# Optimization experiments

Hardware: AMD Instinct MI355X
Metric: run time of the kernel (lower is better)

The kernel has to match this reference:

```python
import jax, jax.numpy as jnp
import numpy as np

B, L, G, HID, H, D = 2, 4096, 256, 768, 12, 64
R = 127            # local_radius
BLK = R + 1        # block_len = 128
N = L // BLK       # 32 blocks (L divisible by BLK)
W = 2 * R + 1      # 255 local window
V = 32             # relative vocab size


def setup_inputs() -> dict:
    ks = jax.random.split(jax.random.key(0), 40)
    inp = {}
    inp["long_input"] = jax.random.normal(ks[0], (B, L, HID), jnp.float32)
    inp["global_input"] = jax.random.normal(ks[1], (B, G, HID), jnp.float32)
    inp["l2l_att_mask"] = jax.random.randint(ks[2], (B, L, W), 0, 2, jnp.int32)
    inp["g2g_att_mask"] = jax.random.randint(ks[3], (B, G, G), 0, 2, jnp.int32)
    inp["l2g_att_mask"] = jax.random.randint(ks[4], (B, L, G), 0, 2, jnp.int32)
    inp["g2l_att_mask"] = jax.random.randint(ks[5], (B, G, L), 0, 2, jnp.int32)
    inp["l2l_relative_att_ids"] = jax.random.randint(ks[6], (B, L, W), 0, V, jnp.int32)
    inp["g2g_relative_att_ids"] = jax.random.randint(ks[7], (B, G, G), 0, V, jnp.int32)
    inp["l2g_relative_att_ids"] = jax.random.randint(ks[8], (B, L, G), 0, V, jnp.int32)
    inp["g2l_relative_att_ids"] = jax.random.randint(ks[9], (B, G, L), 0, V, jnp.int32)
    i = 10
    for nm in ["q_long", "k_long", "v_long", "q_glob", "k_glob", "v_glob"]:
        inp["w" + nm] = 0.02 * jax.random.normal(ks[i], (HID, H * D), jnp.float32); i += 1
        inp["b" + nm] = jnp.zeros((H * D,), jnp.float32)
    inp["rel_emb_long"] = 0.5 * jax.random.normal(ks[i], (V, H, D), jnp.float32); i += 1
    inp["rel_bias_long"] = jnp.zeros((V, H), jnp.float32)
    inp["rel_emb_glob"] = 0.5 * jax.random.normal(ks[i], (V, H, D), jnp.float32); i += 1
    inp["rel_bias_glob"] = jnp.zeros((V, H), jnp.float32)
    inp["wo_long"] = 0.02 * jax.random.normal(ks[i], (H * D, HID), jnp.float32); i += 1
    inp["bo_long"] = jnp.zeros((HID,), jnp.float32)
    inp["wo_glob"] = 0.02 * jax.random.normal(ks[i], (H * D, HID), jnp.float32); i += 1
    inp["bo_glob"] = jnp.zeros((HID,), jnp.float32)
    return inp


def _expand_local(x):
    """[B, L, W] local-window ids -> blocked [B, N, BLK, 3*BLK] (skew + pad),
    zeroing entries outside the local window or outside the sequence."""
    xb = x.reshape(B, N, BLK, W)
    p = jnp.arange(BLK)[:, None]        # query pos within block
    c = jnp.arange(3 * BLK)[None, :]    # key pos within 3-block window
    r = c - p - 1                       # index into the 2R+1 window
    valid = (r >= 0) & (r < W)
    rc = jnp.clip(r, 0, W - 1)
    out = jnp.take_along_axis(xb, jnp.broadcast_to(rc, (B, N, BLK, 3 * BLK)), axis=-1)
    j = (jnp.arange(N)[:, None, None] - 1) * BLK + c  # absolute key position
    valid_full = valid[None] & (j >= 0) & (j < L)     # [N, BLK, 3*BLK]
    return out * valid_full[None].astype(x.dtype)


def reference(long_input, global_input,
              l2l_att_mask, g2g_att_mask, l2g_att_mask, g2l_att_mask,
              l2l_relative_att_ids, g2g_relative_att_ids,
              l2g_relative_att_ids, g2l_relative_att_ids,
              wq_long, bq_long, wk_long, bk_long, wv_long, bv_long,
              wq_glob, bq_glob, wk_glob, bk_glob, wv_glob, bv_glob,
              rel_emb_long, rel_bias_long, rel_emb_glob, rel_bias_glob,
              wo_long, bo_long, wo_glob, bo_glob):
    scale = 1.0 / jnp.sqrt(jnp.float32(D))

    def proj(x, w, b):
        return (x @ w + b).reshape(x.shape[0], x.shape[1], H, D)

    lq, lk, lv = proj(long_input, wq_long, bq_long), proj(long_input, wk_long, bk_long), proj(long_input, wv_long, bv_long)
    gq, gk, gv = proj(global_input, wq_glob, bq_glob), proj(global_input, wk_glob, bk_glob), proj(global_input, wv_glob, bv_glob)

    # ---- long tokens: blocked local attention fused with side (global) keys ----
    qb = lq.reshape(B, N, BLK, H, D)

    def concat3(x):
        xb = x.reshape(B, N, BLK, H, D)
        pad = jnp.zeros_like(xb[:, :1])
        xp = jnp.concatenate([pad, xb, pad], axis=1)  # [B, N+2, BLK, H, D]
        return jnp.concatenate([xp[:, :-2], xp[:, 1:-1], xp[:, 2:]], axis=2)  # [B,N,3BLK,H,D]

    keys = jnp.concatenate([concat3(lk), jnp.broadcast_to(gk[:, None], (B, N, G, H, D))], axis=2)
    vals = jnp.concatenate([concat3(lv), jnp.broadcast_to(gv[:, None], (B, N, G, H, D))], axis=2)

    mask = jnp.concatenate([_expand_local(l2l_att_mask), l2g_att_mask.reshape(B, N, BLK, G)], axis=-1)
    ids = jnp.concatenate([_expand_local(l2l_relative_att_ids), l2g_relative_att_ids.reshape(B, N, BLK, G)], axis=-1)

    scores = jnp.einsum('bnqhd,bnkhd->bnqkh', qb, keys)
    rel_all = jnp.einsum('bnqhd,rhd->bnqrh', qb, rel_emb_long) + rel_bias_long
    rel = jnp.take_along_axis(rel_all, jnp.broadcast_to(ids[..., None], ids.shape + (H,)), axis=3)
    scores = (scores + rel) * scale
    scores = scores - 10000.0 * (1.0 - mask[..., None].astype(scores.dtype))
    probs = jax.nn.softmax(scores, axis=3)
    long_ctx = jnp.einsum('bnqkh,bnkhd->bnqhd', probs, vals).reshape(B, L, H * D)
    long_out = long_ctx @ wo_long + bo_long

    # ---- global tokens: full attention over [global; long] keys ----
    kf = jnp.concatenate([gk, lk], axis=1)
    vf = jnp.concatenate([gv, lv], axis=1)
    gmask = jnp.concatenate([g2g_att_mask, g2l_att_mask], axis=-1)
    gids = jnp.concatenate([g2g_relative_att_ids, g2l_relative_att_ids], axis=-1)
    gs = jnp.einsum('bqhd,bkhd->bqkh', gq, kf)
    grel_all = jnp.einsum('bqhd,rhd->bqrh', gq, rel_emb_glob) + rel_bias_glob
    grel = jnp.take_along_axis(grel_all, jnp.broadcast_to(gids[..., None], gids.shape + (H,)), axis=2)
    gs = (gs + grel) * scale
    gs = gs - 10000.0 * (1.0 - gmask[..., None].astype(gs.dtype))
    gp = jax.nn.softmax(gs, axis=2)
    glob_ctx = jnp.einsum('bqkh,bkhd->bqhd', gp, vf).reshape(B, G, H * D)
    glob_out = glob_ctx @ wo_glob + bo_glob

    return long_out, glob_out
```

## Files before the change

kernel.cpp:

```cpp
#include <hip/hip_runtime.h>
#include <hip/hip_bf16.h>

typedef unsigned short u16;
typedef unsigned char u8;
typedef unsigned int u32;
typedef __attribute__((ext_vector_type(8))) short bf16x8;
typedef __attribute__((ext_vector_type(4))) float f32x4;

#define BB 2
#define LL 4096
#define GG 256
#define HH 12
#define DD 64
#define NB 32
#define WW 255
#define VV 32
#define NCHUNK 17
#define LKEY 640
#define GKEY 4352
#define WMAT 589824
#define MMAT 294912

#define PKL_BLK 20480
#define PKG_BLK 8704
#define WPR_BLK 1152
#define XPL_BLK 3072
#define XPG_BLK 192
#define MPR_BLK 768

__device__ __forceinline__ float bf2f(u16 u) {
  return __uint_as_float(((unsigned)u) << 16);
}
__device__ __forceinline__ u16 f2bf(float f) {
  unsigned u = __float_as_uint(f);
  u += 0x7FFFu + ((u >> 16) & 1u);
  return (u16)(u >> 16);
}
__device__ __forceinline__ float4 ld4bf(const u16* p) {
  ushort4 q = *reinterpret_cast<const ushort4*>(p);
  return make_float4(bf2f(q.x), bf2f(q.y), bf2f(q.z), bf2f(q.w));
}
__device__ __forceinline__ float ldx1(const void* p, size_t idx, bool f32m) {
  if (f32m) return reinterpret_cast<const float*>(p)[idx];
// ... 26 lines not shown
          const int* __restrict__ m_g2g, const int* __restrict__ m_g2l,
          const int* __restrict__ i_g2g, const int* __restrict__ i_g2l,
          u8* __restrict__ pkl, u8* __restrict__ pkg,
          const void* __restrict__ W0, const void* __restrict__ W1,
          const void* __restrict__ W2, const void* __restrict__ W3,
          const void* __restrict__ W4, const void* __restrict__ W5,
          const void* __restrict__ W6, const void* __restrict__ W7,
          u16* __restrict__ wtq, u16* __restrict__ wto,
          const void* __restrict__ xlin, const void* __restrict__ xgin,
          u16* __restrict__ xl, u16* __restrict__ xg,
          const void* __restrict__ embl, const void* __restrict__ rbl,
          const void* __restrict__ embg, const void* __restrict__ rbg,
          const void* __restrict__ bql, const void* __restrict__ bqg,
          u16* __restrict__ wtrel, float* __restrict__ crel,
          const int* __restrict__ flagp) {
  __shared__ u16 T[64][72];
  const bool f32m = (*flagp != 0);
  const int tid = threadIdx.x;
  const int bid = blockIdx.x;

  if (bid < PKL_BLK) {
    const unsigned idx = (unsigned)bid * 256u + tid;
    const int pos = idx & 63;
    const int lnp = pos >> 2, ktp = pos & 3;
    const int qrow = (idx >> 6) & 127;
    const unsigned rest = idx >> 13;
    const int tile = rest % 10;
    const unsigned bn = rest / 10;
    const int n = bn & 31, b = bn >> 5;
    const int c = (tile << 6) + (ktp << 4) + lnp;
    const unsigned bt = (unsigned)b * LL + (n << 7) + qrow;
// ... 19 lines not shown
    const int tl = rest % 68;
    const unsigned b2q = rest / 68;
    const int b = b2q >> 1, qtp = b2q & 1;
    const int c = (tl << 6) + (ktp << 4) + lnp;
    const int q = (qtp << 7) + qrow;
    int mask, id;
    if (c < 256) {
      const size_t base = ((size_t)b * GG + q) * GG + c;
      mask = m_g2g[base]; id = i_g2g[base];
    } else {
      const size_t base = ((size_t)b * GG + q) * (size_t)LL + (c - 256);
      mask = m_g2l[base]; id = i_g2l[base];
    }
    pkg[idx] = (u8)((id & 31) | ((mask ^ 1) << 7));
  } else if (bid < PKL_BLK + PKG_BLK + WPR_BLK) {
    const int blk = bid - (PKL_BLK + PKG_BLK);
    const int mat = blk / 144;
    const int rem = blk % 144;
    const int n0 = (rem % 12) << 6, k0 = (rem / 12) << 6;
    const void* Wm = (mat == 0) ? W0 : (mat == 1) ? W1 : (mat == 2) ? W2
                     : (mat == 3) ? W3 : (mat == 4) ? W4 : (mat == 5) ? W5
                     : (mat == 6) ? W6 : W7;
    u16* wbase = (mat < 6) ? (wtq + (size_t)mat * WMAT)
                           : (wto + (size_t)(mat - 6) * WMAT);
    {
      const int r = tid >> 2, c0 = (tid & 3) << 4;
      if (f32m) {
        const float* wp = reinterpret_cast<const float*>(Wm) + (size_t)(k0 + r) * 768 + n0 + c0;
        #pragma unroll
        for (int j = 0; j < 16; j += 4) {
          float4 v = *reinterpret_cast<const float4*>(wp + j);
          T[r][c0 + j + 0] = f2bf(v.x); T[r][c0 + j + 1] = f2bf(v.y);
          T[r][c0 + j + 2] = f2bf(v.z); T[r][c0 + j + 3] = f2bf(v.w);
        }
      } else {
        const u16* wp = reinterpret_cast<const u16*>(Wm) + (size_t)(k0 + r) * 768 + n0 + c0;
        *reinterpret_cast<int4*>(&T[r][c0]) = reinterpret_cast<const int4*>(wp)[0];
        *reinterpret_cast<int4*>(&T[r][c0 + 8]) = reinterpret_cast<const int4*>(wp)[1];
      }
    }
    __syncthreads();
    {
      const int n = tid >> 2, kc0 = (tid & 3) << 4;
      u16 buf[16];
      #pragma unroll
      for (int j = 0; j < 16; j++) buf[j] = T[kc0 + j][n];
      u16* op = wbase + (size_t)(n0 + n) * 768 + k0 + kc0;
      *reinterpret_cast<int4*>(op) = *reinterpret_cast<int4*>(buf);
      *reinterpret_cast<int4*>(op + 8) = *reinterpret_cast<int4*>(buf + 8);
    }
  } else if (bid < PKL_BLK + PKG_BLK + WPR_BLK + XPL_BLK + XPG_BLK) {
    const int blk = bid - (PKL_BLK + PKG_BLK + WPR_BLK);
    const void* src;
    u16* dst;
    size_t i;
    if (blk < XPL_BLK) {
      src = xlin; dst = xl;
      i = ((size_t)blk * 256 + tid) << 3;
    } else {
      src = xgin; dst = xg;
      i = ((size_t)(blk - XPL_BLK) * 256 + tid) << 3;
    }
    if (f32m) {
      const float* p = reinterpret_cast<const float*>(src) + i;
      float4 a = *reinterpret_cast<const float4*>(p);
      float4 b = *reinterpret_cast<const float4*>(p + 4);
      u16 o[8] = {f2bf(a.x), f2bf(a.y), f2bf(a.z), f2bf(a.w),
                  f2bf(b.x), f2bf(b.y), f2bf(b.z), f2bf(b.w)};
      *reinterpret_cast<int4*>(dst + i) = *reinterpret_cast<int4*>(o);
    } else {
      *reinterpret_cast<int4*>(dst + i) =
          *reinterpret_cast<const int4*>(reinterpret_cast<const u16*>(src) + i);
    }
  } else {
    const int blk = bid - (PKL_BLK + PKG_BLK + WPR_BLK + XPL_BLK + XPG_BLK);
    const int side = blk / 384;
    const int nl = blk % 384;
    const int h = nl >> 5, r = nl & 31;
    const void* Wq = side ? W3 : W0;
    const void* emb = side ? embg : embl;
    const void* bqv = side ? bqg : bql;
    const void* rbv = side ? rbg : rbl;
    float* ef = reinterpret_cast<float*>(&T[0][0]);
    if (tid < 64) ef[tid] = ldx1(emb, ((size_t)r * HH + h) * DD + tid, f32m);
    __syncthreads();
    #pragma unroll
    for (int ko = 0; ko < 3; ko++) {
      const int k = tid + (ko << 8);
      const size_t base = (size_t)k * 768 + h * 64;
      float a = 0.f;
      if (f32m) {
        const float* wp = reinterpret_cast<const float*>(Wq) + base;
        #pragma unroll
        for (int d = 0; d < 64; d += 4) {
          float4 v = *reinterpret_cast<const float4*>(wp + d);
          a += v.x * ef[d] + v.y * ef[d + 1] + v.z * ef[d + 2] + v.w * ef[d + 3];
        }
      } else {
        const u16* wp = reinterpret_cast<const u16*>(Wq) + base;
        #pragma unroll
        for (int d = 0; d < 64; d += 4) {
          float4 v = ld4bf(wp + d);
          a += v.x * ef[d] + v.y * ef[d + 1] + v.z * ef[d + 2] + v.w * ef[d + 3];
        }
      }
      wtrel[(size_t)side * MMAT + (size_t)nl * 768 + k] = f2bf(0.125f * a);
    }
    if (tid == 0) {
      float s = ldx1(rbv, (size_t)r * HH + h, f32m);
      for (int d = 0; d < 64; d++)
        s += ldx1(bqv, h * 64 + d, f32m) * ef[d];
      crel[side * 384 + nl] = 0.125f * s;
    }
  }
}

#define GEMM_CORE(A_, Wt_, row0_, ncol0_)                                        \
  __shared__ u16 lds[16384];                                                     \
  const int tid = threadIdx.x;                                                   \
  const int w = tid >> 6, l = tid & 63;                                          \
  const int lm = l & 15, quad = l >> 4;                                          \
  const int wr = w >> 1, wc = w & 1;                                             \
  const int rb = (w << 5) + (l >> 3);                                            \
  const int c8 = (l & 7) ^ (l >> 3);                                             \
  const u16* asrc = A_ + (size_t)(row0_ + rb) * 768 + (c8 << 3);                 \
  const u16* bsrc = Wt_ + (size_t)(ncol0_ + rb) * 768 + (c8 << 3);               \
  u16* adst = lds + (w << 11) + (l << 3);                                        \
// ... 139 lines not shown
    #pragma unroll
    for (int mt = 0; mt < 4; mt++)
      #pragma unroll
      for (int r = 0; r < 4; r++) {
        const int grow = row0 + (wr << 6) + (mt << 4) + (quad << 2) + r;
        const float v = acc[mt][nt][r] + bv;
        if (f32m)
          reinterpret_cast<float*>(Cv)[c_off + (size_t)grow * 768 + gcol] = v;
        else
          reinterpret_cast<u16*>(Cv)[c_off + (size_t)grow * 768 + gcol] = f2bf(v);
      }
  }
}

__global__ __launch_bounds__(512)
void lattn(const u16* __restrict__ lq, const u16* __restrict__ lk, const u16* __restrict__ lv,
           const u16* __restrict__ gk, const u16* __restrict__ gv,
           const u32* __restrict__ pkl, const u16* __restrict__ rel,
           u16* __restrict__ lctx) {
  const int fid = blockIdx.x + 12 * (blockIdx.y + (blockIdx.z << 5));
  const int hg = fid >> 3;
  const int h = hg % 12;
  const int fl = (fid & 7) + ((hg / 12) << 3);
  const int n = fl & 31, b = fl >> 5;
  const int tid = threadIdx.x;
  __shared__ u16 Kt[64][72];
  __shared__ u16 Vt[64][74];
  __shared__ u16 Pt[128][76];
  __shared__ u16 Rl[128][36];

  const int lane = tid & 63, wv = tid >> 6;
  const int ln = lane & 15, quad = lane >> 4;
  const int tbase = n << 7;

  {
    const int qr = (wv << 4) + (lane >> 2);
    const int seg = (lane & 3) << 3;
    *reinterpret_cast<int4*>(&Rl[qr][seg]) = *reinterpret_cast<const int4*>(
        rel + ((size_t)(b * LL + tbase + qr)) * 384 + h * 32 + seg);
  }

  bf16x8 aq[2];
  {
    const int t = tbase + (wv << 4) + ln;
    const u16* qp = lq + (((size_t)b * LL + t) * HH + h) * DD + (quad << 3);
    aq[0] = *reinterpret_cast<const bf16x8*>(qp);
    aq[1] = *reinterpret_cast<const bf16x8*>(qp + 32);
  }

  const u32* pk32 = pkl + (size_t)(b * 32 + n) * 20480;
  const int skey = tid >> 3, sdg = (tid & 7) << 3;
  const int scol = ((skey & 15) << 2) | (skey >> 4);

  f32x4 Oacc[4];
  #pragma unroll
  for (int dt = 0; dt < 4; dt++) Oacc[dt] = (f32x4){0.f, 0.f, 0.f, 0.f};
  float lpart[4] = {};

  for (int tile = 0; tile < 10; tile++) {
    const int c0 = tile << 6;
    const bool isg = (tile >= 6);

    float badd[16];
    #pragma unroll
    for (int r = 0; r < 4; r++) {
      const int qrow = (wv << 4) + (quad << 2) + r;
      const u32 pw = pk32[(((tile << 7) + qrow) << 4) + ln];
      #pragma unroll
      for (int kt = 0; kt < 4; kt++) {
        const u32 pb = (pw >> (kt << 3)) & 0xFFu;
        const float rv = bf2f(Rl[qrow][pb & 31]);
        badd[(kt << 2) + r] = (pb & 0x80u) ? (rv - 10000.f) : rv;
      }
    }

    __syncthreads();
    {
      int4 kraw = {0, 0, 0, 0}, vraw = {0, 0, 0, 0};
      if (isg) {
        const size_t base = (((size_t)b * GG + (c0 - 384) + skey) * HH + h) * DD + sdg;
        kraw = *reinterpret_cast<const int4*>(gk + base);
        vraw = *reinterpret_cast<const int4*>(gv + base);
      } else {
        const int jabs = ((n - 1) << 7) + c0 + skey;
        if (jabs >= 0 && jabs < LL) {
          const size_t base = (((size_t)b * LL + jabs) * HH + h) * DD + sdg;
          kraw = *reinterpret_cast<const int4*>(lk + base);
          vraw = *reinterpret_cast<const int4*>(lv + base);
        }
      }
      *reinterpret_cast<int4*>(&Kt[skey][sdg]) = kraw;
      u16 vb[8];
      *reinterpret_cast<int4*>(vb) = vraw;
      #pragma unroll
      for (int j = 0; j < 8; j++) Vt[sdg + j][scol] = vb[j];
    }
    __syncthreads();

    f32x4 Sacc[4];
    #pragma unroll
    for (int kt = 0; kt < 4; kt++) Sacc[kt] = (f32x4){0.f, 0.f, 0.f, 0.f};
    __builtin_amdgcn_s_setprio(1);
    #pragma unroll
    for (int kk = 0; kk < 2; kk++) {
      bf16x8 bk[4];
      #pragma unroll
      for (int kt = 0; kt < 4; kt++)
        bk[kt] = *reinterpret_cast<const bf16x8*>(&Kt[(kt << 4) + ln][(kk << 5) + (quad << 3)]);
      #pragma unroll
      for (int kt = 0; kt < 4; kt++)
        Sacc[kt] = __builtin_amdgcn_mfma_f32_16x16x32_bf16(aq[kk], bk[kt], Sacc[kt], 0, 0, 0);
    }
    __builtin_amdgcn_s_setprio(0);

    #pragma unroll
    for (int r = 0; r < 4; r++) {
      const int ql = (wv << 4) + (quad << 2) + r;
      const float p0 = __expf(Sacc[0][r] + badd[0 + r]);
      const float p1 = __expf(Sacc[1][r] + badd[4 + r]);
      const float p2 = __expf(Sacc[2][r] + badd[8 + r]);
      const float p3 = __expf(Sacc[3][r] + badd[12 + r]);
      u32 w0, w1;
      asm("v_cvt_pk_bf16_f32 %0, %1, %2" : "=v"(w0) : "v"(p0), "v"(p1));
      asm("v_cvt_pk_bf16_f32 %0, %1, %2" : "=v"(w1) : "v"(p2), "v"(p3));
      uint2 wp; wp.x = w0; wp.y = w1;
      *reinterpret_cast<uint2*>(&Pt[ql][ln << 2]) = wp;
      lpart[r] += (p0 + p1) + (p2 + p3);
    }

    __builtin_amdgcn_s_setprio(1);
    #pragma unroll
    for (int kk = 0; kk < 2; kk++) {
      bf16x8 ap = *reinterpret_cast<const bf16x8*>(&Pt[(wv << 4) + ln][(kk << 5) + (quad << 3)]);
      #pragma unroll
      for (int dt = 0; dt < 4; dt++) {
        bf16x8 bv = *reinterpret_cast<const bf16x8*>(&Vt[(dt << 4) + ln][(kk << 5) + (quad << 3)]);
        Oacc[dt] = __builtin_amdgcn_mfma_f32_16x16x32_bf16(ap, bv, Oacc[dt], 0, 0, 0);
      }
    }
    __builtin_amdgcn_s_setprio(0);
  }

  #pragma unroll
  for (int r = 0; r < 4; r++) {
    float v = lpart[r];
    v += __shfl_xor(v, 1); v += __shfl_xor(v, 2);
    v += __shfl_xor(v, 4); v += __shfl_xor(v, 8);
    const float inv = 1.0f / v;
    const int t = tbase + (wv << 4) + (quad << 2) + r;
    const size_t base = (((size_t)b * LL + t) * HH + h) * DD;
    #pragma unroll
    for (int dt = 0; dt < 4; dt++)
      lctx[base + (dt << 4) + ln] = f2bf(Oacc[dt][r] * inv);
  }
}

__global__ __launch_bounds__(512)
void gattn(const u16* __restrict__ gq, const u16* __restrict__ gk, const u16* __restrict__ gv,
           const u16* __restrict__ lk, const u16* __restrict__ lv,
           const u32* __restrict__ pkg, const u16* __restrict__ relg,
           float* __restrict__ po, float* __restrict__ pl) {
  const int fid = blockIdx.x;
  const int x = fid & 7;
  const int slot = fid >> 3;
  const int qtp = slot & 1;
  const int g = ((slot >> 1) << 3) | x;
  const int h = g % 12;
  const int cb = g / 12;
  const int chunk = cb % 17;
  const int b = cb / 17;
  const int tid = threadIdx.x;
  __shared__ u16 Kt[64][72];
  __shared__ u16 Vt[64][74];
  __shared__ u16 Pt[128][76];
  __shared__ u16 Rg[128][36];

  const int lane = tid & 63, wv = tid >> 6;
  const int ln = lane & 15, quad = lane >> 4;
  const int qbase = qtp << 7;
  const int kbase = chunk << 8;
  const bool isgg = (chunk == 0);

  {
    const int qr = (wv << 4) + (lane >> 2);
    const int seg = (lane & 3) << 3;
    *reinterpret_cast<int4*>(&Rg[qr][seg]) = *reinterpret_cast<const int4*>(
        relg + ((size_t)(b * GG + qbase + qr)) * 384 + h * 32 + seg);
  }

  bf16x8 aq[2];
  {
    const int qa = qbase + (wv << 4) + ln;
    const u16* qp = gq + (((size_t)b * GG + qa) * HH + h) * DD + (quad << 3);
    aq[0] = *reinterpret_cast<const bf16x8*>(qp);
    aq[1] = *reinterpret_cast<const bf16x8*>(qp + 32);
  }

  const u32* pk32 = pkg + (size_t)((b << 1) + qtp) * 139264;
  const int skey = tid >> 3, sdg = (tid & 7) << 3;
  const int scol = ((skey & 15) << 2) | (skey >> 4);

  f32x4 Oacc[4];
  #pragma unroll
  for (int dt = 0; dt < 4; dt++) Oacc[dt] = (f32x4){0.f, 0.f, 0.f, 0.f};
  float lpart[4] = {};

  for (int tile = 0; tile < 4; tile++) {
    const int tl = (chunk << 2) + tile;

    float badd[16];
    #pragma unroll
    for (int r = 0; r < 4; r++) {
      const int qrow = (wv << 4) + (quad << 2) + r;
      const u32 pw = pk32[(((tl << 7) + qrow) << 4) + ln];
      #pragma unroll
      for (int kt = 0; kt < 4; kt++) {
        const u32 pb = (pw >> (kt << 3)) & 0xFFu;
        const float rv = bf2f(Rg[qrow][pb & 31]);
        badd[(kt << 2) + r] = (pb & 0x80u) ? (rv - 10000.f) : rv;
      }
    }

    __syncthreads();
    {
      const int kc = kbase + (tile << 6) + skey;
      int4 kraw, vraw;
      if (isgg) {
        const size_t base = (((size_t)b * GG + kc) * HH + h) * DD + sdg;
        kraw = *reinterpret_cast<const int4*>(gk + base);
        vraw = *reinterpret_cast<const int4*>(gv + base);
      } else {
        const size_t base = (((size_t)b * LL + (kc - 256)) * HH + h) * DD + sdg;
        kraw = *reinterpret_cast<const int4*>(lk + base);
        vraw = *reinterpret_cast<const int4*>(lv + base);
      }
      *reinterpret_cast<int4*>(&Kt[skey][sdg]) = kraw;
      u16 vb[8];
      *reinterpret_cast<int4*>(vb) = vraw;
      #pragma unroll
      for (int j = 0; j < 8; j++) Vt[sdg + j][scol] = vb[j];
    }
    __syncthreads();

    f32x4 Sacc[4];
    #pragma unroll
    for (int kt = 0; kt < 4; kt++) Sacc[kt] = (f32x4){0.f, 0.f, 0.f, 0.f};
    __builtin_amdgcn_s_setprio(1);
    #pragma unroll
    for (int kk = 0; kk < 2; kk++) {
      bf16x8 bk[4];
      #pragma unroll
      for (int kt = 0; kt < 4; kt++)
        bk[kt] = *reinterpret_cast<const bf16x8*>(&Kt[(kt << 4) + ln][(kk << 5) + (quad << 3)]);
      #pragma unroll
      for (int kt = 0; kt < 4; kt++)
        Sacc[kt] = __builtin_amdgcn_mfma_f32_16x16x32_bf16(aq[kk], bk[kt], Sacc[kt], 0, 0, 0);
    }
    __builtin_amdgcn_s_setprio(0);

    #pragma unroll
    for (int r = 0; r < 4; r++) {
      const int ql = (wv << 4) + (quad << 2) + r;
      const float p0 = __expf(Sacc[0][r] + badd[0 + r]);
      const float p1 = __expf(Sacc[1][r] + badd[4 + r]);
      const float p2 = __expf(Sacc[2][r] + badd[8 + r]);
      const float p3 = __expf(Sacc[3][r] + badd[12 + r]);
      u32 w0, w1;
      asm("v_cvt_pk_bf16_f32 %0, %1, %2" : "=v"(w0) : "v"(p0), "v"(p1));
      asm("v_cvt_pk_bf16_f32 %0, %1, %2" : "=v"(w1) : "v"(p2), "v"(p3));
      uint2 wp; wp.x = w0; wp.y = w1;
      *reinterpret_cast<uint2*>(&Pt[ql][ln << 2]) = wp;
      lpart[r] += (p0 + p1) + (p2 + p3);
    }

    __builtin_amdgcn_s_setprio(1);
    #pragma unroll
    for (int kk = 0; kk < 2; kk++) {
      bf16x8 ap = *reinterpret_cast<const bf16x8*>(&Pt[(wv << 4) + ln][(kk << 5) + (quad << 3)]);
      #pragma unroll
      for (int dt = 0; dt < 4; dt++) {
        bf16x8 bv = *reinterpret_cast<const bf16x8*>(&Vt[(dt << 4) + ln][(kk << 5) + (quad << 3)]);
        Oacc[dt] = __builtin_amdgcn_mfma_f32_16x16x32_bf16(ap, bv, Oacc[dt], 0, 0, 0);
      }
    }
    __builtin_amdgcn_s_setprio(0);
  }

  #pragma unroll
  for (int r = 0; r < 4; r++) {
    float v = lpart[r];
    v += __shfl_xor(v, 1); v += __shfl_xor(v, 2);
    v += __shfl_xor(v, 4); v += __shfl_xor(v, 8);
    const int qa = qbase + (wv << 4) + (quad << 2) + r;
    if (ln == 0)
      pl[(((size_t)chunk * BB + b) * HH + h) * GG + qa] = v;
    const size_t base = ((((size_t)chunk * BB + b) * HH + h) * GG + qa) * DD;
    #pragma unroll
    for (int dt = 0; dt < 4; dt++)
      po[base + (dt << 4) + ln] = Oacc[dt][r];
  }
}

__global__ __launch_bounds__(256)
void gcombine(const float* __restrict__ po, const float* __restrict__ pl,
              u16* __restrict__ gctx) {
  const int flat = blockIdx.x * 256 + threadIdx.x;
  const int d = flat & 63;
  const int rest = flat >> 6;
  const int h = rest % HH;
  const int bq = rest / HH;
  const int b = bq >> 8, qg = bq & 255;
  float so = 0.f, sl = 0.f;
  #pragma unroll
  for (int c = 0; c < NCHUNK; c++) {
// ... 33 lines not shown
  constexpr size_t NRL = (size_t)BB * LL * HH * VV;
  constexpr size_t NRG = (size_t)BB * GG * HH * VV;
  u16* lqw  = reinterpret_cast<u16*>(d_ws);
  u16* lkw  = lqw + NLQ;
  u16* lvw  = lkw + NLQ;
  u16* gqw  = lvw + NLQ;
  u16* gkw  = gqw + NG;
  u16* gvw  = gkw + NG;
  u16* rell = gvw + NG;
  u16* relg = rell + NRL;
  u16* lctx = relg + NRG;
  u16* gctx = lctx + NLQ;
  int* flag = reinterpret_cast<int*>(gctx + NG);
  float* po = reinterpret_cast<float*>(flag + 16);
  float* pl = po + (size_t)NCHUNK * BB * HH * GG * DD;
  u8* pk_l = reinterpret_cast<u8*>(po);
  u16* wt_qkv = reinterpret_cast<u16*>(po) + 2621440;
  u16* xl_bf = lctx;
  u16* xg_bf = gctx;
  u8* pk_g = reinterpret_cast<u8*>(pl + (size_t)NCHUNK * BB * HH * GG);
  u16* wt_o = reinterpret_cast<u16*>(pk_g + (size_t)BB * GG * GKEY);
  u16* wt_rel = wt_o + (size_t)2 * WMAT;
  float* c_rel = reinterpret_cast<float*>(wt_rel + (size_t)2 * MMAT);

  dim3 t256(256);
  detect_dtype<<<1, t256, 0, stream>>>(x_long, flag);
  prep<<<dim3(PKL_BLK + PKG_BLK + WPR_BLK + XPL_BLK + XPG_BLK + MPR_BLK), t256, 0, stream>>>(
      m_l2l, m_l2g, i_l2l, i_l2g, m_g2g, m_g2l, i_g2g, i_g2l, pk_l, pk_g,
      wq_l, wk_l, wv_l, wq_g, wk_g, wv_g, wo_l, wo_g, wt_qkv, wt_o,
      x_long, x_glob, xl_bf, xg_bf,
      rel_emb_l, rel_bias_l, rel_emb_g, rel_bias_g, bq_l, bq_g,
      wt_rel, c_rel, flag);
  gemm_qkv<<<dim3(1428), t256, 0, stream>>>(
      xl_bf, xg_bf, wt_qkv, wt_rel, c_rel,
      bq_l, bk_l, bv_l, bq_g, bk_g, bv_g,
      lqw, lkw, lvw, gqw, gkw, gvw, rell, relg, flag);
  lattn<<<dim3(12, 32, 2), dim3(512), 0, stream>>>(lqw, lkw, lvw, gkw, gvw,
                                                   reinterpret_cast<const u32*>(pk_l), rell, lctx);
  gattn<<<dim3(816), dim3(512), 0, stream>>>(gqw, gkw, gvw, lkw, lvw,
                                             reinterpret_cast<const u32*>(pk_g), relg, po, pl);
  gcombine<<<dim3(1536), t256, 0, stream>>>(po, pl, gctx);
  gemm_out<<<dim3(408), t256, 0, stream>>>(lctx, gctx, wt_o, bo_l, bo_g, d_out, flag);
}
```

Before: 400.9 us.

## Merge local and global attention into one launch and tile rel-weight prep

The separate local and global attention kernels are merged into a single kernel with 1584 blocks. The first 768 blocks do local attention and the rest do global chunked attention, so the two can share the GPU and one launch boundary is removed. The pk_l buffer is moved out of the po region so the concurrent blocks do not overwrite each other's data. The rel-embedding weight prep in the prep kernel is also restructured: it now uses 144 blocks that tile the weight through shared memory in fp32 and compute 8 outputs per thread, instead of 768 blocks that each re-read the full weight slice.

```diff
diff --git a/kernel.cpp b/kernel.cpp
--- a/kernel.cpp
+++ b/kernel.cpp
@@ -26,7 +26,7 @@
 #define WPR_BLK 1152
 #define XPL_BLK 3072
 #define XPG_BLK 192
-#define MPR_BLK 768
+#define MPR_BLK 144
 
 __device__ __forceinline__ float bf2f(u16 u) {
   return __uint_as_float(((unsigned)u) << 16);
@@ -83,7 +83,7 @@
           const void* __restrict__ bql, const void* __restrict__ bqg,
           u16* __restrict__ wtrel, float* __restrict__ crel,
           const int* __restrict__ flagp) {
-  __shared__ u16 T[64][72];
+  __shared__ float SH[6720];
   const bool f32m = (*flagp != 0);
   const int tid = threadIdx.x;
   const int bid = blockIdx.x;
@@ -133,6 +133,7 @@
     }
     pkg[idx] = (u8)((id & 31) | ((mask ^ 1) << 7));
   } else if (bid < PKL_BLK + PKG_BLK + WPR_BLK) {
+    u16* T16 = reinterpret_cast<u16*>(SH);
     const int blk = bid - (PKL_BLK + PKG_BLK);
     const int mat = blk / 144;
     const int rem = blk % 144;
@@ -149,13 +150,13 @@
         #pragma unroll
         for (int j = 0; j < 16; j += 4) {
           float4 v = *reinterpret_cast<const float4*>(wp + j);
-          T[r][c0 + j + 0] = f2bf(v.x); T[r][c0 + j + 1] = f2bf(v.y);
-          T[r][c0 + j + 2] = f2bf(v.z); T[r][c0 + j + 3] = f2bf(v.w);
+          T16[r * 72 + c0 + j + 0] = f2bf(v.x); T16[r * 72 + c0 + j + 1] = f2bf(v.y);
+          T16[r * 72 + c0 + j + 2] = f2bf(v.z); T16[r * 72 + c0 + j + 3] = f2bf(v.w);
         }
       } else {
         const u16* wp = reinterpret_cast<const u16*>(Wm) + (size_t)(k0 + r) * 768 + n0 + c0;
-        *reinterpret_cast<int4*>(&T[r][c0]) = reinterpret_cast<const int4*>(wp)[0];
-        *reinterpret_cast<int4*>(&T[r][c0 + 8]) = reinterpret_cast<const int4*>(wp)[1];
+        *reinterpret_cast<int4*>(&T16[r * 72 + c0]) = reinterpret_cast<const int4*>(wp)[0];
+        *reinterpret_cast<int4*>(&T16[r * 72 + c0 + 8]) = reinterpret_cast<const int4*>(wp)[1];
       }
     }
     __syncthreads();
@@ -163,7 +164,7 @@
       const int n = tid >> 2, kc0 = (tid & 3) << 4;
       u16 buf[16];
       #pragma unroll
-      for (int j = 0; j < 16; j++) buf[j] = T[kc0 + j][n];
+      for (int j = 0; j < 16; j++) buf[j] = T16[(kc0 + j) * 72 + n];
       u16* op = wbase + (size_t)(n0 + n) * 768 + k0 + kc0;
       *reinterpret_cast<int4*>(op) = *reinterpret_cast<int4*>(buf);
       *reinterpret_cast<int4*>(op + 8) = *reinterpret_cast<int4*>(buf + 8);
@@ -193,43 +194,70 @@
     }
   } else {
     const int blk = bid - (PKL_BLK + PKG_BLK + WPR_BLK + XPL_BLK + XPG_BLK);
-    const int side = blk / 384;
-    const int nl = blk % 384;
-    const int h = nl >> 5, r = nl & 31;
+    const int side = blk / 72;
+    const int rem = blk % 72;
+    const int h = rem / 6, ksp = rem % 6;
+    const int k0 = ksp << 7;
     const void* Wq = side ? W3 : W0;
     const void* emb = side ? embg : embl;
     const void* bqv = side ? bqg : bql;
     const void* rbv = side ? rbg : rbl;
-    float* ef = reinterpret_cast<float*>(&T[0][0]);
-    if (tid < 64) ef[tid] = ldx1(emb, ((size_t)r * HH + h) * DD + tid, f32m);
+    float* Ef = SH;
+    float* Wf = SH + 32 * 68;
+    float* bqf = SH + 32 * 68 + 64 * 68;
+    float* rbf = bqf + 64;
+    {
+      const int r = tid >> 3, d0 = (tid & 7) << 3;
+      #pragma unroll
+      for (int j = 0; j < 8; j++)
+        Ef[r * 68 + d0 + j] = ldx1(emb, ((size_t)r * HH + h) * DD + d0 + j, f32m);
+      if (tid < 64) bqf[tid] = ldx1(bqv, h * 64 + tid, f32m);
+      else if (tid < 96) rbf[tid - 64] = ldx1(rbv, (size_t)(tid - 64) * HH + h, f32m);
+    }
     __syncthreads();
-    #pragma unroll
-    for (int ko = 0; ko < 3; ko++) {
-      const int k = tid + (ko << 8);
-      const size_t base = (size_t)k * 768 + h * 64;
-      float a = 0.f;
-      if (f32m) {
-        const float* wp = reinterpret_cast<const float*>(Wq) + base;
-        #pragma unroll
-        for (int d = 0; d < 64; d += 4) {
-          float4 v = *reinterpret_cast<const float4*>(wp + d);
-          a += v.x * ef[d] + v.y * ef[d + 1] + v.z * ef[d + 2] + v.w * ef[d + 3];
-        }
-      } else {
-        const u16* wp = reinterpret_cast<const u16*>(Wq) + base;
-        #pragma unroll
-        for (int d = 0; d < 64; d += 4) {
-          float4 v = ld4bf(wp + d);
-          a += v.x * ef[d] + v.y * ef[d + 1] + v.z * ef[d + 2] + v.w * ef[d + 3];
-        }
-      }
-      wtrel[(size_t)side * MMAT + (size_t)nl * 768 + k] = f2bf(0.125f * a);
-    }
-    if (tid == 0) {
-      float s = ldx1(rbv, (size_t)r * HH + h, f32m);
-      for (int d = 0; d < 64; d++)
-        s += ldx1(bqv, h * 64 + d, f32m) * ef[d];
-      crel[side * 384 + nl] = 0.125f * s;
+    if (ksp == 0 && tid < 32) {
+      float s = rbf[tid];
+      #pragma unroll 16
+      for (int d = 0; d < 64; d++) s += bqf[d] * Ef[tid * 68 + d];
+      crel[side * 384 + h * 32 + tid] = 0.125f * s;
+    }
+    const int kr = tid >> 2, rg = tid & 3;
+    for (int kt = 0; kt < 2; kt++) {
+      const int kb = k0 + (kt << 6);
+      {
+        const int sr = tid >> 2, d0 = (tid & 3) << 4;
+        const size_t base = (size_t)(kb + sr) * 768 + h * 64 + d0;
+        if (f32m) {
+          const float* wp = reinterpret_cast<const float*>(Wq) + base;
+          #pragma unroll
+          for (int j = 0; j < 16; j += 4)
+            *reinterpret_cast<float4*>(&Wf[sr * 68 + d0 + j]) =
+                *reinterpret_cast<const float4*>(wp + j);
+        } else {
+          const u16* wp = reinterpret_cast<const u16*>(Wq) + base;
+          #pragma unroll
+          for (int j = 0; j < 16; j += 4) {
+            float4 v = ld4bf(wp + j);
+            *reinterpret_cast<float4*>(&Wf[sr * 68 + d0 + j]) = v;
+          }
+        }
+      }
+      __syncthreads();
+      float a[8] = {};
+      #pragma unroll
+      for (int d = 0; d < 64; d += 4) {
+        const float4 wv = *reinterpret_cast<const float4*>(&Wf[kr * 68 + d]);
+        #pragma unroll
+        for (int j = 0; j < 8; j++) {
+          const float4 ev = *reinterpret_cast<const float4*>(&Ef[(rg * 8 + j) * 68 + d]);
+          a[j] += wv.x * ev.x + wv.y * ev.y + wv.z * ev.z + wv.w * ev.w;
+        }
+      }
+      #pragma unroll
+      for (int j = 0; j < 8; j++)
+        wtrel[(size_t)side * MMAT + (size_t)(h * 32 + rg * 8 + j) * 768 + kb + kr] =
+            f2bf(0.125f * a[j]);
+      __syncthreads();
     }
   }
 }
@@ -399,290 +427,278 @@
 }
 
 __global__ __launch_bounds__(512)
-void lattn(const u16* __restrict__ lq, const u16* __restrict__ lk, const u16* __restrict__ lv,
-           const u16* __restrict__ gk, const u16* __restrict__ gv,
-           const u32* __restrict__ pkl, const u16* __restrict__ rel,
-           u16* __restrict__ lctx) {
-  const int fid = blockIdx.x + 12 * (blockIdx.y + (blockIdx.z << 5));
-  const int hg = fid >> 3;
-  const int h = hg % 12;
-  const int fl = (fid & 7) + ((hg / 12) << 3);
-  const int n = fl & 31, b = fl >> 5;
-  const int tid = threadIdx.x;
+void attn(const u16* __restrict__ lq, const u16* __restrict__ lk, const u16* __restrict__ lv,
+          const u16* __restrict__ gq, const u16* __restrict__ gk, const u16* __restrict__ gv,
+          const u32* __restrict__ pkl, const u32* __restrict__ pkg,
+          const u16* __restrict__ rell, const u16* __restrict__ relg,
+          u16* __restrict__ lctx, float* __restrict__ po, float* __restrict__ pl) {
   __shared__ u16 Kt[64][72];
   __shared__ u16 Vt[64][74];
   __shared__ u16 Pt[128][76];
-  __shared__ u16 Rl[128][36];
-
+  __shared__ u16 Rw[128][36];
+
+  const int tid = threadIdx.x;
   const int lane = tid & 63, wv = tid >> 6;
   const int ln = lane & 15, quad = lane >> 4;
-  const int tbase = n << 7;
-
-  {
-    const int qr = (wv << 4) + (lane >> 2);
-    const int seg = (lane & 3) << 3;
-    *reinterpret_cast<int4*>(&Rl[qr][seg]) = *reinterpret_cast<const int4*>(
-        rel + ((size_t)(b * LL + tbase + qr)) * 384 + h * 32 + seg);
-  }
-
-  bf16x8 aq[2];
-  {
-    const int t = tbase + (wv << 4) + ln;
-    const u16* qp = lq + (((size_t)b * LL + t) * HH + h) * DD + (quad << 3);
-    aq[0] = *reinterpret_cast<const bf16x8*>(qp);
-    aq[1] = *reinterpret_cast<const bf16x8*>(qp + 32);
-  }
-
-  const u32* pk32 = pkl + (size_t)(b * 32 + n) * 20480;
   const int skey = tid >> 3, sdg = (tid & 7) << 3;
   const int scol = ((skey & 15) << 2) | (skey >> 4);
 
-  f32x4 Oacc[4];
-  #pragma unroll
-  for (int dt = 0; dt < 4; dt++) Oacc[dt] = (f32x4){0.f, 0.f, 0.f, 0.f};
-  float lpart[4] = {};
-
-  for (int tile = 0; tile < 10; tile++) {
-    const int c0 = tile << 6;
-    const bool isg = (tile >= 6);
-
-    float badd[16];
+  if (blockIdx.x < 768) {
+    const int fid = blockIdx.x;
+    const int hg = fid >> 3;
+    const int h = hg % 12;
+    const int fl = (fid & 7) + ((hg / 12) << 3);
+    const int n = fl & 31, b = fl >> 5;
+    const int tbase = n << 7;
+
+    {
+      const int qr = (wv << 4) + (lane >> 2);
+      const int seg = (lane & 3) << 3;
+      *reinterpret_cast<int4*>(&Rw[qr][seg]) = *reinterpret_cast<const int4*>(
+          rell + ((size_t)(b * LL + tbase + qr)) * 384 + h * 32 + seg);
+    }
+
+    bf16x8 aq[2];
+    {
+      const int t = tbase + (wv << 4) + ln;
+      const u16* qp = lq + (((size_t)b * LL + t) * HH + h) * DD + (quad << 3);
+      aq[0] = *reinterpret_cast<const bf16x8*>(qp);
+      aq[1] = *reinterpret_cast<const bf16x8*>(qp + 32);
+    }
+
+    const u32* pk32 = pkl + (size_t)(b * 32 + n) * 20480;
+
+    f32x4 Oacc[4];
+    #pragma unroll
+    for (int dt = 0; dt < 4; dt++) Oacc[dt] = (f32x4){0.f, 0.f, 0.f, 0.f};
+    float lpart[4] = {};
+
+    for (int tile = 0; tile < 10; tile++) {
+      const int c0 = tile << 6;
+      const bool isg = (tile >= 6);
+
+      float badd[16];
+      #pragma unroll
+      for (int r = 0; r < 4; r++) {
+        const int qrow = (wv << 4) + (quad << 2) + r;
+        const u32 pw = pk32[(((tile << 7) + qrow) << 4) + ln];
+        #pragma unroll
+        for (int kt = 0; kt < 4; kt++) {
+          const u32 pb = (pw >> (kt << 3)) & 0xFFu;
+          const float rv = bf2f(Rw[qrow][pb & 31]);
+          badd[(kt << 2) + r] = (pb & 0x80u) ? (rv - 10000.f) : rv;
+        }
+      }
+
+      __syncthreads();
+      {
+        int4 kraw = {0, 0, 0, 0}, vraw = {0, 0, 0, 0};
+        if (isg) {
+          const size_t base = (((size_t)b * GG + (c0 - 384) + skey) * HH + h) * DD + sdg;
+          kraw = *reinterpret_cast<const int4*>(gk + base);
+          vraw = *reinterpret_cast<const int4*>(gv + base);
+        } else {
+          const int jabs = ((n - 1) << 7) + c0 + skey;
+          if (jabs >= 0 && jabs < LL) {
+            const size_t base = (((size_t)b * LL + jabs) * HH + h) * DD + sdg;
+            kraw = *reinterpret_cast<const int4*>(lk + base);
+            vraw = *reinterpret_cast<const int4*>(lv + base);
+          }
+        }
+        *reinterpret_cast<int4*>(&Kt[skey][sdg]) = kraw;
+        u16 vb[8];
+        *reinterpret_cast<int4*>(vb) = vraw;
+        #pragma unroll
+        for (int j = 0; j < 8; j++) Vt[sdg + j][scol] = vb[j];
+      }
+      __syncthreads();
+
+      f32x4 Sacc[4];
+      #pragma unroll
+      for (int kt = 0; kt < 4; kt++) Sacc[kt] = (f32x4){0.f, 0.f, 0.f, 0.f};
+      __builtin_amdgcn_s_setprio(1);
+      #pragma unroll
+      for (int kk = 0; kk < 2; kk++) {
+        bf16x8 bk[4];
+        #pragma unroll
+        for (int kt = 0; kt < 4; kt++)
+          bk[kt] = *reinterpret_cast<const bf16x8*>(&Kt[(kt << 4) + ln][(kk << 5) + (quad << 3)]);
+        #pragma unroll
+        for (int kt = 0; kt < 4; kt++)
+          Sacc[kt] = __builtin_amdgcn_mfma_f32_16x16x32_bf16(aq[kk], bk[kt], Sacc[kt], 0, 0, 0);
+      }
+      __builtin_amdgcn_s_setprio(0);
+
+      #pragma unroll
+      for (int r = 0; r < 4; r++) {
+        const int ql = (wv << 4) + (quad << 2) + r;
+        const float p0 = __expf(Sacc[0][r] + badd[0 + r]);
+        const float p1 = __expf(Sacc[1][r] + badd[4 + r]);
+        const float p2 = __expf(Sacc[2][r] + badd[8 + r]);
+        const float p3 = __expf(Sacc[3][r] + badd[12 + r]);
+        u32 w0, w1;
+        asm("v_cvt_pk_bf16_f32 %0, %1, %2" : "=v"(w0) : "v"(p0), "v"(p1));
+        asm("v_cvt_pk_bf16_f32 %0, %1, %2" : "=v"(w1) : "v"(p2), "v"(p3));
+        uint2 wp; wp.x = w0; wp.y = w1;
+        *reinterpret_cast<uint2*>(&Pt[ql][ln << 2]) = wp;
+        lpart[r] += (p0 + p1) + (p2 + p3);
+      }
+
+      __builtin_amdgcn_s_setprio(1);
+      #pragma unroll
+      for (int kk = 0; kk < 2; kk++) {
+        bf16x8 ap = *reinterpret_cast<const bf16x8*>(&Pt[(wv << 4) + ln][(kk << 5) + (quad << 3)]);
+        #pragma unroll
+        for (int dt = 0; dt < 4; dt++) {
+          bf16x8 bv = *reinterpret_cast<const bf16x8*>(&Vt[(dt << 4) + ln][(kk << 5) + (quad << 3)]);
+          Oacc[dt] = __builtin_amdgcn_mfma_f32_16x16x32_bf16(ap, bv, Oacc[dt], 0, 0, 0);
+        }
+      }
+      __builtin_amdgcn_s_setprio(0);
+    }
+
     #pragma unroll
     for (int r = 0; r < 4; r++) {
-      const int qrow = (wv << 4) + (quad << 2) + r;
-      const u32 pw = pk32[(((tile << 7) + qrow) << 4) + ln];
-      #pragma unroll
-      for (int kt = 0; kt < 4; kt++) {
-        const u32 pb = (pw >> (kt << 3)) & 0xFFu;
-        const float rv = bf2f(Rl[qrow][pb & 31]);
-        badd[(kt << 2) + r] = (pb & 0x80u) ? (rv - 10000.f) : rv;
-      }
-    }
-
-    __syncthreads();
+      float v = lpart[r];
+      v += __shfl_xor(v, 1); v += __shfl_xor(v, 2);
+      v += __shfl_xor(v, 4); v += __shfl_xor(v, 8);
+      const float inv = 1.0f / v;
+      const int t = tbase + (wv << 4) + (quad << 2) + r;
+      const size_t base = (((size_t)b * LL + t) * HH + h) * DD;
+      #pragma unroll
+      for (int dt = 0; dt < 4; dt++)
+        lctx[base + (dt << 4) + ln] = f2bf(Oacc[dt][r] * inv);
+    }
+  } else {
+    const int fid = blockIdx.x - 768;
+    const int x = fid & 7;
+    const int slot = fid >> 3;
+    const int qtp = slot & 1;
+    const int g = ((slot >> 1) << 3) | x;
+    const int h = g % 12;
+    const int cb = g / 12;
+    const int chunk = cb % 17;
+    const int b = cb / 17;
+    const int qbase = qtp << 7;
+    const int kbase = chunk << 8;
+    const bool isgg = (chunk == 0);
+
     {
-      int4 kraw = {0, 0, 0, 0}, vraw = {0, 0, 0, 0};
-      if (isg) {
-        const size_t base = (((size_t)b * GG + (c0 - 384) + skey) * HH + h) * DD + sdg;
-        kraw = *reinterpret_cast<const int4*>(gk + base);
-        vraw = *reinterpret_cast<const int4*>(gv + base);
-      } else {
-        const int jabs = ((n - 1) << 7) + c0 + skey;
-        if (jabs >= 0 && jabs < LL) {
-          const size_t base = (((size_t)b * LL + jabs) * HH + h) * DD + sdg;
+      const int qr = (wv << 4) + (lane >> 2);
+      const int seg = (lane & 3) << 3;
+      *reinterpret_cast<int4*>(&Rw[qr][seg]) = *reinterpret_cast<const int4*>(
+          relg + ((size_t)(b * GG + qbase + qr)) * 384 + h * 32 + seg);
+    }
+
+    bf16x8 aq[2];
+    {
+      const int qa = qbase + (wv << 4) + ln;
+      const u16* qp = gq + (((size_t)b * GG + qa) * HH + h) * DD + (quad << 3);
+      aq[0] = *reinterpret_cast<const bf16x8*>(qp);
+      aq[1] = *reinterpret_cast<const bf16x8*>(qp + 32);
+    }
+
+    const u32* pk32 = pkg + (size_t)((b << 1) + qtp) * 139264;
+
+    f32x4 Oacc[4];
+    #pragma unroll
+    for (int dt = 0; dt < 4; dt++) Oacc[dt] = (f32x4){0.f, 0.f, 0.f, 0.f};
+    float lpart[4] = {};
+
+    for (int tile = 0; tile < 4; tile++) {
+      const int tl = (chunk << 2) + tile;
+
+      float badd[16];
+      #pragma unroll
+      for (int r = 0; r < 4; r++) {
+        const int qrow = (wv << 4) + (quad << 2) + r;
+        const u32 pw = pk32[(((tl << 7) + qrow) << 4) + ln];
+        #pragma unroll
+        for (int kt = 0; kt < 4; kt++) {
+          const u32 pb = (pw >> (kt << 3)) & 0xFFu;
+          const float rv = bf2f(Rw[qrow][pb & 31]);
+          badd[(kt << 2) + r] = (pb & 0x80u) ? (rv - 10000.f) : rv;
+        }
+      }
+
+      __syncthreads();
+      {
+        const int kc = kbase + (tile << 6) + skey;
+        int4 kraw, vraw;
+        if (isgg) {
+          const size_t base = (((size_t)b * GG + kc) * HH + h) * DD + sdg;
+          kraw = *reinterpret_cast<const int4*>(gk + base);
+          vraw = *reinterpret_cast<const int4*>(gv + base);
+        } else {
+          const size_t base = (((size_t)b * LL + (kc - 256)) * HH + h) * DD + sdg;
           kraw = *reinterpret_cast<const int4*>(lk + base);
           vraw = *reinterpret_cast<const int4*>(lv + base);
         }
-      }
-      *reinterpret_cast<int4*>(&Kt[skey][sdg]) = kraw;
-      u16 vb[8];
-      *reinterpret_cast<int4*>(vb) = vraw;
-      #pragma unroll
-      for (int j = 0; j < 8; j++) Vt[sdg + j][scol] = vb[j];
-    }
-    __syncthreads();
-
-    f32x4 Sacc[4];
-    #pragma unroll
-    for (int kt = 0; kt < 4; kt++) Sacc[kt] = (f32x4){0.f, 0.f, 0.f, 0.f};
-    __builtin_amdgcn_s_setprio(1);
-    #pragma unroll
-    for (int kk = 0; kk < 2; kk++) {
-      bf16x8 bk[4];
-      #pragma unroll
-      for (int kt = 0; kt < 4; kt++)
-        bk[kt] = *reinterpret_cast<const bf16x8*>(&Kt[(kt << 4) + ln][(kk << 5) + (quad << 3)]);
-      #pragma unroll
-      for (int kt = 0; kt < 4; kt++)
-        Sacc[kt] = __builtin_amdgcn_mfma_f32_16x16x32_bf16(aq[kk], bk[kt], Sacc[kt], 0, 0, 0);
-    }
-    __builtin_amdgcn_s_setprio(0);
+        *reinterpret_cast<int4*>(&Kt[skey][sdg]) = kraw;
+        u16 vb[8];
+        *reinterpret_cast<int4*>(vb) = vraw;
+        #pragma unroll
+        for (int j = 0; j < 8; j++) Vt[sdg + j][scol] = vb[j];
+      }
+      __syncthreads();
+
+      f32x4 Sacc[4];
+      #pragma unroll
+      for (int kt = 0; kt < 4; kt++) Sacc[kt] = (f32x4){0.f, 0.f, 0.f, 0.f};
+      __builtin_amdgcn_s_setprio(1);
+      #pragma unroll
+      for (int kk = 0; kk < 2; kk++) {
+        bf16x8 bk[4];
+        #pragma unroll
+        for (int kt = 0; kt < 4; kt++)
+          bk[kt] = *reinterpret_cast<const bf16x8*>(&Kt[(kt << 4) + ln][(kk << 5) + (quad << 3)]);
+        #pragma unroll
+        for (int kt = 0; kt < 4; kt++)
+          Sacc[kt] = __builtin_amdgcn_mfma_f32_16x16x32_bf16(aq[kk], bk[kt], Sacc[kt], 0, 0, 0);
+      }
+      __builtin_amdgcn_s_setprio(0);
+
+      #pragma unroll
+      for (int r = 0; r < 4; r++) {
+        const int ql = (wv << 4) + (quad << 2) + r;
+        const float p0 = __expf(Sacc[0][r] + badd[0 + r]);
+        const float p1 = __expf(Sacc[1][r] + badd[4 + r]);
+        const float p2 = __expf(Sacc[2][r] + badd[8 + r]);
+        const float p3 = __expf(Sacc[3][r] + badd[12 + r]);
+        u32 w0, w1;
+        asm("v_cvt_pk_bf16_f32 %0, %1, %2" : "=v"(w0) : "v"(p0), "v"(p1));
+        asm("v_cvt_pk_bf16_f32 %0, %1, %2" : "=v"(w1) : "v"(p2), "v"(p3));
+        uint2 wp; wp.x = w0; wp.y = w1;
+        *reinterpret_cast<uint2*>(&Pt[ql][ln << 2]) = wp;
+        lpart[r] += (p0 + p1) + (p2 + p3);
+      }
+
+      __builtin_amdgcn_s_setprio(1);
+      #pragma unroll
+      for (int kk = 0; kk < 2; kk++) {
+        bf16x8 ap = *reinterpret_cast<const bf16x8*>(&Pt[(wv << 4) + ln][(kk << 5) + (quad << 3)]);
+        #pragma unroll
+        for (int dt = 0; dt < 4; dt++) {
+          bf16x8 bv = *reinterpret_cast<const bf16x8*>(&Vt[(dt << 4) + ln][(kk << 5) + (quad << 3)]);
+          Oacc[dt] = __builtin_amdgcn_mfma_f32_16x16x32_bf16(ap, bv, Oacc[dt], 0, 0, 0);
+        }
+      }
+      __builtin_amdgcn_s_setprio(0);
+    }
 
     #pragma unroll
     for (int r = 0; r < 4; r++) {
-      const int ql = (wv << 4) + (quad << 2) + r;
-      const float p0 = __expf(Sacc[0][r] + badd[0 + r]);
-      const float p1 = __expf(Sacc[1][r] + badd[4 + r]);
-      const float p2 = __expf(Sacc[2][r] + badd[8 + r]);
-      const float p3 = __expf(Sacc[3][r] + badd[12 + r]);
-      u32 w0, w1;
-      asm("v_cvt_pk_bf16_f32 %0, %1, %2" : "=v"(w0) : "v"(p0), "v"(p1));
-      asm("v_cvt_pk_bf16_f32 %0, %1, %2" : "=v"(w1) : "v"(p2), "v"(p3));
-      uint2 wp; wp.x = w0; wp.y = w1;
-      *reinterpret_cast<uint2*>(&Pt[ql][ln << 2]) = wp;
-      lpart[r] += (p0 + p1) + (p2 + p3);
-    }
-
-    __builtin_amdgcn_s_setprio(1);
-    #pragma unroll
-    for (int kk = 0; kk < 2; kk++) {
-      bf16x8 ap = *reinterpret_cast<const bf16x8*>(&Pt[(wv << 4) + ln][(kk << 5) + (quad << 3)]);
-      #pragma unroll
-      for (int dt = 0; dt < 4; dt++) {
-        bf16x8 bv = *reinterpret_cast<const bf16x8*>(&Vt[(dt << 4) + ln][(kk << 5) + (quad << 3)]);
-        Oacc[dt] = __builtin_amdgcn_mfma_f32_16x16x32_bf16(ap, bv, Oacc[dt], 0, 0, 0);
-      }
-    }
-    __builtin_amdgcn_s_setprio(0);
-  }
-
-  #pragma unroll
-  for (int r = 0; r < 4; r++) {
-    float v = lpart[r];
-    v += __shfl_xor(v, 1); v += __shfl_xor(v, 2);
-    v += __shfl_xor(v, 4); v += __shfl_xor(v, 8);
-    const float inv = 1.0f / v;
-    const int t = tbase + (wv << 4) + (quad << 2) + r;
-    const size_t base = (((size_t)b * LL + t) * HH + h) * DD;
-    #pragma unroll
-    for (int dt = 0; dt < 4; dt++)
-      lctx[base + (dt << 4) + ln] = f2bf(Oacc[dt][r] * inv);
-  }
-}
-
-__global__ __launch_bounds__(512)
-void gattn(const u16* __restrict__ gq, const u16* __restrict__ gk, const u16* __restrict__ gv,
-           const u16* __restrict__ lk, const u16* __restrict__ lv,
-           const u32* __restrict__ pkg, const u16* __restrict__ relg,
-           float* __restrict__ po, float* __restrict__ pl) {
-  const int fid = blockIdx.x;
-  const int x = fid & 7;
-  const int slot = fid >> 3;
-  const int qtp = slot & 1;
-  const int g = ((slot >> 1) << 3) | x;
-  const int h = g % 12;
-  const int cb = g / 12;
-  const int chunk = cb % 17;
-  const int b = cb / 17;
-  const int tid = threadIdx.x;
-  __shared__ u16 Kt[64][72];
-  __shared__ u16 Vt[64][74];
-  __shared__ u16 Pt[128][76];
-  __shared__ u16 Rg[128][36];
-
-  const int lane = tid & 63, wv = tid >> 6;
-  const int ln = lane & 15, quad = lane >> 4;
-  const int qbase = qtp << 7;
-  const int kbase = chunk << 8;
-  const bool isgg = (chunk == 0);
-
-  {
-    const int qr = (wv << 4) + (lane >> 2);
-    const int seg = (lane & 3) << 3;
-    *reinterpret_cast<int4*>(&Rg[qr][seg]) = *reinterpret_cast<const int4*>(
-        relg + ((size_t)(b * GG + qbase + qr)) * 384 + h * 32 + seg);
-  }
-
-  bf16x8 aq[2];
-  {
-    const int qa = qbase + (wv << 4) + ln;
-    const u16* qp = gq + (((size_t)b * GG + qa) * HH + h) * DD + (quad << 3);
-    aq[0] = *reinterpret_cast<const bf16x8*>(qp);
-    aq[1] = *reinterpret_cast<const bf16x8*>(qp + 32);
-  }
-
-  const u32* pk32 = pkg + (size_t)((b << 1) + qtp) * 139264;
-  const int skey = tid >> 3, sdg = (tid & 7) << 3;
-  const int scol = ((skey & 15) << 2) | (skey >> 4);
-
-  f32x4 Oacc[4];
-  #pragma unroll
-  for (int dt = 0; dt < 4; dt++) Oacc[dt] = (f32x4){0.f, 0.f, 0.f, 0.f};
-  float lpart[4] = {};
-
-  for (int tile = 0; tile < 4; tile++) {
-    const int tl = (chunk << 2) + tile;
-
-    float badd[16];
-    #pragma unroll
-    for (int r = 0; r < 4; r++) {
-      const int qrow = (wv << 4) + (quad << 2) + r;
-      const u32 pw = pk32[(((tl << 7) + qrow) << 4) + ln];
-      #pragma unroll
-      for (int kt = 0; kt < 4; kt++) {
-        const u32 pb = (pw >> (kt << 3)) & 0xFFu;
-        const float rv = bf2f(Rg[qrow][pb & 31]);
-        badd[(kt << 2) + r] = (pb & 0x80u) ? (rv - 10000.f) : rv;
-      }
-    }
-
-    __syncthreads();
-    {
-      const int kc = kbase + (tile << 6) + skey;
-      int4 kraw, vraw;
-      if (isgg) {
-        const size_t base = (((size_t)b * GG + kc) * HH + h) * DD + sdg;
-        kraw = *reinterpret_cast<const int4*>(gk + base);
-        vraw = *reinterpret_cast<const int4*>(gv + base);
-      } else {
-        const size_t base = (((size_t)b * LL + (kc - 256)) * HH + h) * DD + sdg;
-        kraw = *reinterpret_cast<const int4*>(lk + base);
-        vraw = *reinterpret_cast<const int4*>(lv + base);
-      }
-      *reinterpret_cast<int4*>(&Kt[skey][sdg]) = kraw;
-      u16 vb[8];
-      *reinterpret_cast<int4*>(vb) = vraw;
-      #pragma unroll
-      for (int j = 0; j < 8; j++) Vt[sdg + j][scol] = vb[j];
-    }
-    __syncthreads();
-
-    f32x4 Sacc[4];
-    #pragma unroll
-    for (int kt = 0; kt < 4; kt++) Sacc[kt] = (f32x4){0.f, 0.f, 0.f, 0.f};
-    __builtin_amdgcn_s_setprio(1);
-    #pragma unroll
-    for (int kk = 0; kk < 2; kk++) {
-      bf16x8 bk[4];
-      #pragma unroll
-      for (int kt = 0; kt < 4; kt++)
-        bk[kt] = *reinterpret_cast<const bf16x8*>(&Kt[(kt << 4) + ln][(kk << 5) + (quad << 3)]);
-      #pragma unroll
-      for (int kt = 0; kt < 4; kt++)
-        Sacc[kt] = __builtin_amdgcn_mfma_f32_16x16x32_bf16(aq[kk], bk[kt], Sacc[kt], 0, 0, 0);
-    }
-    __builtin_amdgcn_s_setprio(0);
-
-    #pragma unroll
-    for (int r = 0; r < 4; r++) {
-      const int ql = (wv << 4) + (quad << 2) + r;
-      const float p0 = __expf(Sacc[0][r] + badd[0 + r]);
-      const float p1 = __expf(Sacc[1][r] + badd[4 + r]);
-      const float p2 = __expf(Sacc[2][r] + badd[8 + r]);
-      const float p3 = __expf(Sacc[3][r] + badd[12 + r]);
-      u32 w0, w1;
-      asm("v_cvt_pk_bf16_f32 %0, %1, %2" : "=v"(w0) : "v"(p0), "v"(p1));
-      asm("v_cvt_pk_bf16_f32 %0, %1, %2" : "=v"(w1) : "v"(p2), "v"(p3));
-      uint2 wp; wp.x = w0; wp.y = w1;
-      *reinterpret_cast<uint2*>(&Pt[ql][ln << 2]) = wp;
-      lpart[r] += (p0 + p1) + (p2 + p3);
-    }
-
-    __builtin_amdgcn_s_setprio(1);
-    #pragma unroll
-    for (int kk = 0; kk < 2; kk++) {
-      bf16x8 ap = *reinterpret_cast<const bf16x8*>(&Pt[(wv << 4) + ln][(kk << 5) + (quad << 3)]);
-      #pragma unroll
-      for (int dt = 0; dt < 4; dt++) {
-        bf16x8 bv = *reinterpret_cast<const bf16x8*>(&Vt[(dt << 4) + ln][(kk << 5) + (quad << 3)]);
-        Oacc[dt] = __builtin_amdgcn_mfma_f32_16x16x32_bf16(ap, bv, Oacc[dt], 0, 0, 0);
-      }
-    }
-    __builtin_amdgcn_s_setprio(0);
-  }
-
-  #pragma unroll
-  for (int r = 0; r < 4; r++) {
-    float v = lpart[r];
-    v += __shfl_xor(v, 1); v += __shfl_xor(v, 2);
-    v += __shfl_xor(v, 4); v += __shfl_xor(v, 8);
-    const int qa = qbase + (wv << 4) + (quad << 2) + r;
-    if (ln == 0)
-      pl[(((size_t)chunk * BB + b) * HH + h) * GG + qa] = v;
-    const size_t base = ((((size_t)chunk * BB + b) * HH + h) * GG + qa) * DD;
-    #pragma unroll
-    for (int dt = 0; dt < 4; dt++)
-      po[base + (dt << 4) + ln] = Oacc[dt][r];
+      float v = lpart[r];
+      v += __shfl_xor(v, 1); v += __shfl_xor(v, 2);
+      v += __shfl_xor(v, 4); v += __shfl_xor(v, 8);
+      const int qa = qbase + (wv << 4) + (quad << 2) + r;
+      if (ln == 0)
+        pl[(((size_t)chunk * BB + b) * HH + h) * GG + qa] = v;
+      const size_t base = ((((size_t)chunk * BB + b) * HH + h) * GG + qa) * DD;
+      #pragma unroll
+      for (int dt = 0; dt < 4; dt++)
+        po[base + (dt << 4) + ln] = Oacc[dt][r];
+    }
   }
 }
 
@@ -746,12 +762,12 @@
   int* flag = reinterpret_cast<int*>(gctx + NG);
   float* po = reinterpret_cast<float*>(flag + 16);
   float* pl = po + (size_t)NCHUNK * BB * HH * GG * DD;
-  u8* pk_l = reinterpret_cast<u8*>(po);
   u16* wt_qkv = reinterpret_cast<u16*>(po) + 2621440;
   u16* xl_bf = lctx;
   u16* xg_bf = gctx;
   u8* pk_g = reinterpret_cast<u8*>(pl + (size_t)NCHUNK * BB * HH * GG);
-  u16* wt_o = reinterpret_cast<u16*>(pk_g + (size_t)BB * GG * GKEY);
+  u8* pk_l = pk_g + (size_t)BB * GG * GKEY;
+  u16* wt_o = reinterpret_cast<u16*>(pk_l + (size_t)BB * LL * LKEY);
   u16* wt_rel = wt_o + (size_t)2 * WMAT;
   float* c_rel = reinterpret_cast<float*>(wt_rel + (size_t)2 * MMAT);
 
@@ -767,10 +783,10 @@
       xl_bf, xg_bf, wt_qkv, wt_rel, c_rel,
       bq_l, bk_l, bv_l, bq_g, bk_g, bv_g,
       lqw, lkw, lvw, gqw, gkw, gvw, rell, relg, flag);
-  lattn<<<dim3(12, 32, 2), dim3(512), 0, stream>>>(lqw, lkw, lvw, gkw, gvw,
-                                                   reinterpret_cast<const u32*>(pk_l), rell, lctx);
-  gattn<<<dim3(816), dim3(512), 0, stream>>>(gqw, gkw, gvw, lkw, lvw,
-                                             reinterpret_cast<const u32*>(pk_g), relg, po, pl);
+  attn<<<dim3(1584), dim3(512), 0, stream>>>(
+      lqw, lkw, lvw, gqw, gkw, gvw,
+      reinterpret_cast<const u32*>(pk_l), reinterpret_cast<const u32*>(pk_g),
+      rell, relg, lctx, po, pl);
   gcombine<<<dim3(1536), t256, 0, stream>>>(po, pl, gctx);
   gemm_out<<<dim3(408), t256, 0, stream>>>(lctx, gctx, wt_o, bo_l, bo_g, d_out, flag);
 }
```

New measurement: 373.4 us. 1.07x faster.
